# Kernel tuning notes

Measured on AMD Instinct MI355X. Metric: run time of the kernel, lower is better.

The kernel has to match this reference:

```python
import jax, jax.numpy as jnp
import numpy as np

T = 10          # time_steps
IN_DIM = 784    # 28*28
HID = 256
NCLS = 47
THRESH = 1.0
TAU_MEM = 2.0   # LIF membrane time constant
TAU_OUT = 2.0   # readout EMA time constant


@jax.custom_vjp
def spike_fn(u):
    # Heaviside spike on (v - threshold), surrogate gradient in bwd.
    return (u >= 0.0).astype(u.dtype)

def _spike_fwd(u):
    return spike_fn(u), u

def _spike_bwd(u, g):
    # sigmoid surrogate derivative, slope 4
    s = jax.nn.sigmoid(4.0 * u)
    return (g * 4.0 * s * (1.0 - s),)

spike_fn.defvjp(_spike_fwd, _spike_bwd)


def setup_inputs() -> dict:
    key = jax.random.key(0)
    k1, k2, k3 = jax.random.split(key, 3)
    x = jax.random.uniform(k1, (4096, 1, 28, 28), dtype=jnp.float32)
    W1 = jax.random.normal(k2, (IN_DIM, HID), dtype=jnp.float32) / np.float32(np.sqrt(IN_DIM))
    b1 = jnp.zeros((HID,), jnp.float32)
    Wr = jax.random.normal(k3, (HID, NCLS), dtype=jnp.float32) / np.float32(np.sqrt(HID))
    br = jnp.zeros((NCLS,), jnp.float32)
    return {"x": x, "W1": W1, "b1": b1, "Wr": Wr, "br": br}


def reference(x, W1, b1, Wr, br):
    B = x.shape[0]
    xf = x.reshape(B, -1)  # [B, 784] pixel intensities in [0,1]
    # rate_encode_flat: Bernoulli(p=pixel) spikes per timestep -> [T, B, 784]
    ek = jax.random.key(42)
    seq = (jax.random.uniform(ek, (T, B, IN_DIM), dtype=xf.dtype) < xf[None]).astype(xf.dtype)

    def step(carry, s_t):
        v_hid, v_out = carry
        I_hid = s_t @ W1 + b1                      # [B, HID]
        v_hid = v_hid + (I_hid - v_hid) / TAU_MEM  # leaky integration
        spk = spike_fn(v_hid - THRESH)             # spike emission
        v_hid = v_hid * (1.0 - spk)                # hard reset to 0
        I = spk @ Wr + br                          # [B, NCLS]
        v_out = v_out + (I - v_out) / TAU_OUT      # output EMA
        return (v_hid, v_out), None

    init = (jnp.zeros((B, HID), xf.dtype), jnp.zeros((B, NCLS), xf.dtype))
    (_, v_out), _ = jax.lax.scan(step, init, seq)
    return v_out
```

## Files before the change

kernel.cpp:

```cpp
#include <hip/hip_runtime.h>
#include <stdint.h>


#define T_STEPS 10
#define BATCH   4096
#define IN_DIM  784
#define HID     256
#define NCLS    47
#define NROWS   (T_STEPS * BATCH)
#define KWORDS  25
#define KPAD    800
#define M_TILE  160

#define WS_IALL_OFF 0u
#define WS_SPK_OFF  41943040u
#define WS_W1HI_OFF 46039040u
#define WS_W1MD_OFF (46039040u + 409600u)
#define WS_W1LO_OFF (46039040u + 819200u)

typedef __attribute__((ext_vector_type(8))) short    bf16x8;
typedef __attribute__((ext_vector_type(4))) float    f32x4;
typedef __attribute__((ext_vector_type(4))) uint32_t u32x4;

__device__ __forceinline__ uint32_t rotl32(uint32_t x, uint32_t r) {
    return __builtin_amdgcn_alignbit(x, x, 32u - r);
}

__device__ __forceinline__ uint32_t tf_hash(uint32_t lo) {
    const uint32_t ks1 = 42u;
    const uint32_t ks2 = 0x1BD11BDAu ^ 42u;
    uint32_t x0 = 0u;
    uint32_t x1 = lo + ks1;
#define TF_RND(r) { x0 += x1; x1 = rotl32(x1, r); x1 ^= x0; }
    TF_RND(13) TF_RND(15) TF_RND(26) TF_RND(6)
    x0 += ks1; x1 += ks2 + 1u;
    TF_RND(17) TF_RND(29) TF_RND(16) TF_RND(24)
    x0 += ks2; x1 += 2u;
    TF_RND(13) TF_RND(15) TF_RND(26) TF_RND(6)
    x1 += ks1 + 3u;
    TF_RND(17) TF_RND(29) TF_RND(16) TF_RND(24)
    x0 += ks1; x1 += ks2 + 4u;
    TF_RND(13) TF_RND(15) TF_RND(26) TF_RND(6)
    x0 += ks2; x1 += 5u;
#undef TF_RND
    return x0 ^ x1;
}

__global__ __launch_bounds__(256) void splitk_k(
        const float* __restrict__ W1, ushort* __restrict__ hiT,
        ushort* __restrict__ midT, ushort* __restrict__ loT) {
    int n = blockIdx.x;
    for (int k = threadIdx.x; k < KPAD; k += 256) {
        float w = (k < IN_DIM) ? W1[k * HID + n] : 0.0f;
        uint32_t u = __float_as_uint(w);
        uint32_t hb = (u + 0x7FFFu + ((u >> 16) & 1u)) >> 16;
        float hf = __uint_as_float(hb << 16);
        float r1 = w - hf;
        uint32_t u1 = __float_as_uint(r1);
        uint32_t mb = (u1 + 0x7FFFu + ((u1 >> 16) & 1u)) >> 16;
        float mf2 = __uint_as_float(mb << 16);
        float r2 = r1 - mf2;
        uint32_t u2 = __float_as_uint(r2);
        uint32_t lb = (u2 + 0x7FFFu + ((u2 >> 16) & 1u)) >> 16;
        hiT [n * KPAD + k] = (ushort)hb;
        midT[n * KPAD + k] = (ushort)mb;
        loT [n * KPAD + k] = (ushort)lb;
    }
}

__global__ __launch_bounds__(256) void spikegen_k(
        const float* __restrict__ x, uint32_t* __restrict__ spk) {
    const int kw  = blockIdx.y;
    const int row = (blockIdx.x << 8) + threadIdx.x;
    const int b   = row & (BATCH - 1);
    const int k0  = kw << 5;
    const float* xp = x + (size_t)b * IN_DIM + k0;
    const uint32_t ib = (uint32_t)row * (uint32_t)IN_DIM + (uint32_t)k0;
    uint32_t wbits = 0u;
#define SPIKE_G(g) { \
    float4 xa = *(const float4*)(xp + ((g) << 3)); \
    float4 xb = *(const float4*)(xp + ((g) << 3) + 4); \
    uint32_t base = ib + (uint32_t)((g) << 3); \
    uint32_t bits = 0u; \
    bits |= ((float)(tf_hash(base + 0u) >> 9) < xa.x * 8388608.0f) ? 1u   : 0u; \
    bits |= ((float)(tf_hash(base + 1u) >> 9) < xa.y * 8388608.0f) ? 2u   : 0u; \
    bits |= ((float)(tf_hash(base + 2u) >> 9) < xa.z * 8388608.0f) ? 4u   : 0u; \
    bits |= ((float)(tf_hash(base + 3u) >> 9) < xa.w * 8388608.0f) ? 8u   : 0u; \
    bits |= ((float)(tf_hash(base + 4u) >> 9) < xb.x * 8388608.0f) ? 16u  : 0u; \
    bits |= ((float)(tf_hash(base + 5u) >> 9) < xb.y * 8388608.0f) ? 32u  : 0u; \
    bits |= ((float)(tf_hash(base + 6u) >> 9) < xb.z * 8388608.0f) ? 64u  : 0u; \
    bits |= ((float)(tf_hash(base + 7u) >> 9) < xb.w * 8388608.0f) ? 128u : 0u; \
    wbits |= bits << ((g) << 3); }
    if (kw != KWORDS - 1) {
        SPIKE_G(0) SPIKE_G(1) SPIKE_G(2) SPIKE_G(3)
    } else {
        SPIKE_G(0) SPIKE_G(1)
    }
#undef SPIKE_G
    spk[(size_t)kw * NROWS + row] = wbits;
}

#define LDS_AB0 0
#define LDS_B0  20480
#define B_BUFSZ 49152
#define A_BUFSZ 10240

__global__ __launch_bounds__(512, 2) void fused_gemm_k(
        const ushort* __restrict__ hiT, const ushort* __restrict__ midT,
        const ushort* __restrict__ loT, const float* __restrict__ b1,
        const uint32_t* __restrict__ spk, float* __restrict__ I_all) {
    __shared__ __align__(16) char lds[118784];

    const int tid = threadIdx.x;
    const int l   = tid & 63;
    const int wv  = tid >> 6;
    const int wm  = wv >> 2;
    const int wn  = wv & 3;
    const int m0  = blockIdx.x * M_TILE;

    f32x4 acc[5][4] = {};

    const int q   = l >> 4;
    const int sig = q ^ (l & 3) ^ ((l >> 2) & 3);
    const int a_rd = wm * 5120 + ((l & 15) << 6) + (sig << 4);
    const int b_rd = (((wn << 6) + (l & 15)) << 6) + (sig << 4);

    const ushort* hi_p[2];
    const ushort* md_p[2];
    const ushort* lo_p[2];
    int bdst[2];
#pragma unroll
    for (int i = 0; i < 2; ++i) {
        int s  = (i << 9) + tid;
        int n  = s >> 2;
        int qs = s & 3;
        int qd = qs ^ (n & 3) ^ ((n >> 2) & 3);
        size_t eoff = (size_t)n * KPAD + ((size_t)qd << 3);
        hi_p[i] = hiT  + eoff;
        md_p[i] = midT + eoff;
        lo_p[i] = loT  + eoff;
        bdst[i] = ((i << 9) + (wv << 6)) << 4;
    }

    const int  eq   = tid & 3;
    const int  r1   = tid >> 2;
    const bool has2 = (tid < 128);
    const int  r2   = 128 + (tid >> 2);
    const int  ea1  = (r1 << 6) + ((eq ^ (r1 & 3) ^ ((r1 >> 2) & 3)) << 4);
    const int  ea2  = (r2 << 6) + ((eq ^ (r2 & 3) ^ ((r2 >> 2) & 3)) << 4);

    const uint32_t* sp1 = spk + (size_t)(m0 + r1);
    const uint32_t* sp2 = spk + (size_t)(m0 + (has2 ? r2 : r1));

#define SPIKE_FRAG_STORE(byt, dst) { \
    u32x4 v_; \
    v_.x = (((byt) & 1u)   ? 0x3F80u : 0u) | (((byt) & 2u)   ? 0x3F800000u : 0u); \
    v_.y = (((byt) & 4u)   ? 0x3F80u : 0u) | (((byt) & 8u)   ? 0x3F800000u : 0u); \
    v_.z = (((byt) & 16u)  ? 0x3F80u : 0u) | (((byt) & 32u)  ? 0x3F800000u : 0u); \
    v_.w = (((byt) & 64u)  ? 0x3F80u : 0u) | (((byt) & 128u) ? 0x3F800000u : 0u); \
    *(u32x4*)(dst) = v_; }

#define STAGE_B(koff, bbase) \
    _Pragma("unroll") \
    for (int i = 0; i < 2; ++i) { \
        __builtin_amdgcn_global_load_lds( \
            (const __attribute__((address_space(1))) void*)(hi_p[i] + (koff)), \
            (__attribute__((address_space(3))) void*)(lds + (bbase) + bdst[i]), \
            16, 0, 0); \
        __builtin_amdgcn_global_load_lds( \
            (const __attribute__((address_space(1))) void*)(md_p[i] + (koff)), \
            (__attribute__((address_space(3))) void*)(lds + (bbase) + 16384 + bdst[i]), \
            16, 0, 0); \
        __builtin_amdgcn_global_load_lds( \
            (const __attribute__((address_space(1))) void*)(lo_p[i] + (koff)), \
            (__attribute__((address_space(3))) void*)(lds + (bbase) + 32768 + bdst[i]), \
            16, 0, 0); \
    }

    uint32_t w1c = sp1[0];
    uint32_t w2c = has2 ? sp2[0] : 0u;
    STAGE_B(0, LDS_B0)
    SPIKE_FRAG_STORE((w1c >> (eq << 3)) & 0xffu, lds + ea1)
    if (has2) SPIKE_FRAG_STORE((w2c >> (eq << 3)) & 0xffu, lds + ea2)
    uint32_t w1n = sp1[NROWS];
    uint32_t w2n = has2 ? sp2[NROWS] : 0u;
    __syncthreads();

    int cur = 0;
#pragma unroll 1
    for (int kw = 0; kw < KWORDS; ++kw) {
        const int nxt = cur ^ 1;
        if (kw < KWORDS - 1) {
            const int koff = (kw + 1) << 5;
            STAGE_B(koff, LDS_B0 + nxt * B_BUFSZ)
            SPIKE_FRAG_STORE((w1n >> (eq << 3)) & 0xffu,
                             lds + nxt * A_BUFSZ + ea1)
            if (has2) SPIKE_FRAG_STORE((w2n >> (eq << 3)) & 0xffu,
                                       lds + nxt * A_BUFSZ + ea2)
            if (kw < KWORDS - 2) {
                w1n = sp1[(size_t)(kw + 2) * NROWS];
                if (has2) w2n = sp2[(size_t)(kw + 2) * NROWS];
            }
        }

        const char* A = lds + cur * A_BUFSZ;
        const char* B = lds + LDS_B0 + cur * B_BUFSZ;
        bf16x8 af[5];
#pragma unroll
        for (int mt = 0; mt < 5; ++mt)
            af[mt] = *(const bf16x8*)(A + a_rd + (mt << 10));
#pragma unroll
        for (int nt = 0; nt < 4; ++nt) {
            bf16x8 bh = *(const bf16x8*)(B + b_rd + (nt << 10));
            bf16x8 bm = *(const bf16x8*)(B + 16384 + b_rd + (nt << 10));
            bf16x8 bl = *(const bf16x8*)(B + 32768 + b_rd + (nt << 10));
#pragma unroll
            for (int mt = 0; mt < 5; ++mt) {
                acc[mt][nt] = __builtin_amdgcn_mfma_f32_16x16x32_bf16(af[mt], bh, acc[mt][nt], 0, 0, 0);
                acc[mt][nt] = __builtin_amdgcn_mfma_f32_16x16x32_bf16(af[mt], bm, acc[mt][nt], 0, 0, 0);
                acc[mt][nt] = __builtin_amdgcn_mfma_f32_16x16x32_bf16(af[mt], bl, acc[mt][nt], 0, 0, 0);
            }
        }

        __syncthreads();
        cur = nxt;
    }
#undef STAGE_B
#undef SPIKE_FRAG_STORE

    const int c0 = l & 15;
    float b1v[4];
#pragma unroll
    for (int nt = 0; nt < 4; ++nt)
        b1v[nt] = b1[(wn << 6) + (nt << 4) + c0];
#pragma unroll
    for (int mt = 0; mt < 5; ++mt) {
#pragma unroll
        for (int nt = 0; nt < 4; ++nt) {
            int col = (wn << 6) + (nt << 4) + c0;
#pragma unroll
            for (int r = 0; r < 4; ++r) {
                int row = m0 + wm * 80 + (mt << 4) + (q << 2) + r;
                I_all[(size_t)row * HID + col] = acc[mt][nt][r] + b1v[nt];
            }
        }
    }
}

__global__ __launch_bounds__(256) void scanout_k(
        const float* __restrict__ I_all, const float* __restrict__ Wr,
        const float* __restrict__ br, float* __restrict__ out) {
    __shared__ float gl[4 * 256];
    const int tid = threadIdx.x;
    const int b0  = blockIdx.x << 2;

#pragma unroll
    for (int b = 0; b < 4; ++b) {
        const float* p = I_all + ((size_t)(b0 + b) << 8) + tid;
        float v = 0.f, ga = 0.f, wt = 0.0009765625f;
#pragma unroll
        for (int t = 0; t < T_STEPS; ++t) {
            float I = p[(size_t)t * BATCH * HID];
            v = v + (I - v) * 0.5f;
            if (v >= 1.0f) { ga += wt; v = 0.f; }
            wt += wt;
        }
        gl[(b << 8) + tid] = ga;
    }
    __syncthreads();

    const int wv = tid >> 6;
    const int c  = tid & 63;
    if (c >= NCLS) return;
    const float* gb = &gl[wv << 8];
    float acc = 0.f;
    for (int h4 = 0; h4 < 64; ++h4) {
        float w0 = Wr[((h4 << 2) + 0) * NCLS + c];
        float w1 = Wr[((h4 << 2) + 1) * NCLS + c];
        float w2 = Wr[((h4 << 2) + 2) * NCLS + c];
        float w3 = Wr[((h4 << 2) + 3) * NCLS + c];
        float4 gg = *(const float4*)&gb[h4 << 2];
        acc = fmaf(gg.x, w0, acc);
        acc = fmaf(gg.y, w1, acc);
        acc = fmaf(gg.z, w2, acc);
        acc = fmaf(gg.w, w3, acc);
    }
    float brv = br[c] * 0.9990234375f;
    out[(b0 + wv) * NCLS + c] = acc + brv;
}

extern "C" void kernel_launch(void* const* d_in, const int* in_sizes, int n_in,
                              void* d_out, int out_size, void* d_ws, size_t ws_size,
                              hipStream_t stream) {
    const float* x  = (const float*)d_in[0];
    const float* W1 = (const float*)d_in[1];
    const float* b1 = (const float*)d_in[2];
    const float* Wr = (const float*)d_in[3];
    const float* br = (const float*)d_in[4];
    float* out = (float*)d_out;

    float*    I_all = (float*)   ((char*)d_ws + WS_IALL_OFF);
    uint32_t* spkw  = (uint32_t*)((char*)d_ws + WS_SPK_OFF);
    ushort*   w1hi  = (ushort*)  ((char*)d_ws + WS_W1HI_OFF);
    ushort*   w1md  = (ushort*)  ((char*)d_ws + WS_W1MD_OFF);
    ushort*   w1lo  = (ushort*)  ((char*)d_ws + WS_W1LO_OFF);

    splitk_k<<<HID, 256, 0, stream>>>(W1, w1hi, w1md, w1lo);
    spikegen_k<<<dim3(NROWS / 256, KWORDS), 256, 0, stream>>>(x, spkw);
    fused_gemm_k<<<NROWS / M_TILE, 512, 0, stream>>>(w1hi, w1md, w1lo, b1, spkw, I_all);
    scanout_k<<<BATCH / 4, 256, 0, stream>>>(I_all, Wr, br, out);
}
```

Measured before the change: 192.0 us.

## Fuse Bernoulli spike generation into the GEMM kernel, dropping spikegen pass

Removes the separate spike-generation kernel and its packed-bitmask workspace. Each GEMM thread now computes the Threefry hash for its 8-element spike fragment inline while staging the next K-slice. This saves a kernel launch and the global write and read of the spike words. In exchange, the hash ALU work is interleaved with the MFMA loop, which can lengthen the critical path and raise register pressure in the GEMM.

```diff
diff --git a/kernel.cpp b/kernel.cpp
--- a/kernel.cpp
+++ b/kernel.cpp
@@ -13,7 +13,6 @@
 #define M_TILE  160
 
 #define WS_IALL_OFF 0u
-#define WS_SPK_OFF  41943040u
 #define WS_W1HI_OFF 46039040u
 #define WS_W1MD_OFF (46039040u + 409600u)
 #define WS_W1LO_OFF (46039040u + 819200u)
@@ -44,6 +43,21 @@
     x0 += ks2; x1 += 5u;
 #undef TF_RND
     return x0 ^ x1;
+}
+
+__device__ __forceinline__ uint32_t hash8(uint32_t ib, const float* xp) {
+    float4 xa = *(const float4*)xp;
+    float4 xb = *(const float4*)(xp + 4);
+    uint32_t bits = 0u;
+    bits |= ((float)(tf_hash(ib + 0u) >> 9) < xa.x * 8388608.0f) ? 1u   : 0u;
+    bits |= ((float)(tf_hash(ib + 1u) >> 9) < xa.y * 8388608.0f) ? 2u   : 0u;
+    bits |= ((float)(tf_hash(ib + 2u) >> 9) < xa.z * 8388608.0f) ? 4u   : 0u;
+    bits |= ((float)(tf_hash(ib + 3u) >> 9) < xa.w * 8388608.0f) ? 8u   : 0u;
+    bits |= ((float)(tf_hash(ib + 4u) >> 9) < xb.x * 8388608.0f) ? 16u  : 0u;
+    bits |= ((float)(tf_hash(ib + 5u) >> 9) < xb.y * 8388608.0f) ? 32u  : 0u;
+    bits |= ((float)(tf_hash(ib + 6u) >> 9) < xb.z * 8388608.0f) ? 64u  : 0u;
+    bits |= ((float)(tf_hash(ib + 7u) >> 9) < xb.w * 8388608.0f) ? 128u : 0u;
+    return bits;
 }
 
 __global__ __launch_bounds__(256) void splitk_k(
@@ -68,39 +82,6 @@
     }
 }
 
-__global__ __launch_bounds__(256) void spikegen_k(
-        const float* __restrict__ x, uint32_t* __restrict__ spk) {
-    const int kw  = blockIdx.y;
-    const int row = (blockIdx.x << 8) + threadIdx.x;
-    const int b   = row & (BATCH - 1);
-    const int k0  = kw << 5;
-    const float* xp = x + (size_t)b * IN_DIM + k0;
-    const uint32_t ib = (uint32_t)row * (uint32_t)IN_DIM + (uint32_t)k0;
-    uint32_t wbits = 0u;
-#define SPIKE_G(g) { \
-    float4 xa = *(const float4*)(xp + ((g) << 3)); \
-    float4 xb = *(const float4*)(xp + ((g) << 3) + 4); \
-    uint32_t base = ib + (uint32_t)((g) << 3); \
-    uint32_t bits = 0u; \
-    bits |= ((float)(tf_hash(base + 0u) >> 9) < xa.x * 8388608.0f) ? 1u   : 0u; \
-    bits |= ((float)(tf_hash(base + 1u) >> 9) < xa.y * 8388608.0f) ? 2u   : 0u; \
-    bits |= ((float)(tf_hash(base + 2u) >> 9) < xa.z * 8388608.0f) ? 4u   : 0u; \
-    bits |= ((float)(tf_hash(base + 3u) >> 9) < xa.w * 8388608.0f) ? 8u   : 0u; \
-    bits |= ((float)(tf_hash(base + 4u) >> 9) < xb.x * 8388608.0f) ? 16u  : 0u; \
-    bits |= ((float)(tf_hash(base + 5u) >> 9) < xb.y * 8388608.0f) ? 32u  : 0u; \
-    bits |= ((float)(tf_hash(base + 6u) >> 9) < xb.z * 8388608.0f) ? 64u  : 0u; \
-    bits |= ((float)(tf_hash(base + 7u) >> 9) < xb.w * 8388608.0f) ? 128u : 0u; \
-    wbits |= bits << ((g) << 3); }
-    if (kw != KWORDS - 1) {
-        SPIKE_G(0) SPIKE_G(1) SPIKE_G(2) SPIKE_G(3)
-    } else {
-        SPIKE_G(0) SPIKE_G(1)
-    }
-#undef SPIKE_G
-    spk[(size_t)kw * NROWS + row] = wbits;
-}
-
-#define LDS_AB0 0
 #define LDS_B0  20480
 #define B_BUFSZ 49152
 #define A_BUFSZ 10240
@@ -108,7 +89,7 @@
 __global__ __launch_bounds__(512, 2) void fused_gemm_k(
         const ushort* __restrict__ hiT, const ushort* __restrict__ midT,
         const ushort* __restrict__ loT, const float* __restrict__ b1,
-        const uint32_t* __restrict__ spk, float* __restrict__ I_all) {
+        const float* __restrict__ x, float* __restrict__ I_all) {
     __shared__ __align__(16) char lds[118784];
 
     const int tid = threadIdx.x;
@@ -149,8 +130,12 @@
     const int  ea1  = (r1 << 6) + ((eq ^ (r1 & 3) ^ ((r1 >> 2) & 3)) << 4);
     const int  ea2  = (r2 << 6) + ((eq ^ (r2 & 3) ^ ((r2 >> 2) & 3)) << 4);
 
-    const uint32_t* sp1 = spk + (size_t)(m0 + r1);
-    const uint32_t* sp2 = spk + (size_t)(m0 + (has2 ? r2 : r1));
+    const int rg1 = m0 + r1;
+    const int rg2 = m0 + (has2 ? r2 : r1);
+    const float*   xp1 = x + (size_t)(rg1 & (BATCH - 1)) * IN_DIM + (eq << 3);
+    const float*   xp2 = x + (size_t)(rg2 & (BATCH - 1)) * IN_DIM + (eq << 3);
+    const uint32_t ib1 = (uint32_t)rg1 * (uint32_t)IN_DIM + (uint32_t)(eq << 3);
+    const uint32_t ib2 = (uint32_t)rg2 * (uint32_t)IN_DIM + (uint32_t)(eq << 3);
 
 #define SPIKE_FRAG_STORE(byt, dst) { \
     u32x4 v_; \
@@ -177,13 +162,15 @@
             16, 0, 0); \
     }
 
-    uint32_t w1c = sp1[0];
-    uint32_t w2c = has2 ? sp2[0] : 0u;
     STAGE_B(0, LDS_B0)
-    SPIKE_FRAG_STORE((w1c >> (eq << 3)) & 0xffu, lds + ea1)
-    if (has2) SPIKE_FRAG_STORE((w2c >> (eq << 3)) & 0xffu, lds + ea2)
-    uint32_t w1n = sp1[NROWS];
-    uint32_t w2n = has2 ? sp2[NROWS] : 0u;
+    {
+        uint32_t byt1 = hash8(ib1, xp1);
+        SPIKE_FRAG_STORE(byt1, lds + ea1)
+        if (has2) {
+            uint32_t byt2 = hash8(ib2, xp2);
+            SPIKE_FRAG_STORE(byt2, lds + ea2)
+        }
+    }
     __syncthreads();
 
     int cur = 0;
@@ -193,14 +180,14 @@
         if (kw < KWORDS - 1) {
             const int koff = (kw + 1) << 5;
             STAGE_B(koff, LDS_B0 + nxt * B_BUFSZ)
-            SPIKE_FRAG_STORE((w1n >> (eq << 3)) & 0xffu,
-                             lds + nxt * A_BUFSZ + ea1)
-            if (has2) SPIKE_FRAG_STORE((w2n >> (eq << 3)) & 0xffu,
-                                       lds + nxt * A_BUFSZ + ea2)
-            if (kw < KWORDS - 2) {
-                w1n = sp1[(size_t)(kw + 2) * NROWS];
-                if (has2) w2n = sp2[(size_t)(kw + 2) * NROWS];
+            const bool tail = (kw + 1 == KWORDS - 1);
+            uint32_t byt1 = 0u, byt2 = 0u;
+            if (!(tail && eq >= 2)) {
+                byt1 = hash8(ib1 + koff, xp1 + koff);
+                if (has2) byt2 = hash8(ib2 + koff, xp2 + koff);
             }
+            SPIKE_FRAG_STORE(byt1, lds + nxt * A_BUFSZ + ea1)
+            if (has2) SPIKE_FRAG_STORE(byt2, lds + nxt * A_BUFSZ + ea2)
         }
 
         const char* A = lds + cur * A_BUFSZ;
@@ -299,14 +286,12 @@
     const float* br = (const float*)d_in[4];
     float* out = (float*)d_out;
 
-    float*    I_all = (float*)   ((char*)d_ws + WS_IALL_OFF);
-    uint32_t* spkw  = (uint32_t*)((char*)d_ws + WS_SPK_OFF);
-    ushort*   w1hi  = (ushort*)  ((char*)d_ws + WS_W1HI_OFF);
-    ushort*   w1md  = (ushort*)  ((char*)d_ws + WS_W1MD_OFF);
-    ushort*   w1lo  = (ushort*)  ((char*)d_ws + WS_W1LO_OFF);
+    float*  I_all = (float*) ((char*)d_ws + WS_IALL_OFF);
+    ushort* w1hi  = (ushort*)((char*)d_ws + WS_W1HI_OFF);
+    ushort* w1md  = (ushort*)((char*)d_ws + WS_W1MD_OFF);
+    ushort* w1lo  = (ushort*)((char*)d_ws + WS_W1LO_OFF);
 
     splitk_k<<<HID, 256, 0, stream>>>(W1, w1hi, w1md, w1lo);
-    spikegen_k<<<dim3(NROWS / 256, KWORDS), 256, 0, stream>>>(x, spkw);
-    fused_gemm_k<<<NROWS / M_TILE, 512, 0, stream>>>(w1hi, w1md, w1lo, b1, spkw, I_all);
+    fused_gemm_k<<<NROWS / M_TILE, 512, 0, stream>>>(w1hi, w1md, w1lo, b1, x, I_all);
     scanout_k<<<BATCH / 4, 256, 0, stream>>>(I_all, Wr, br, out);
 }
```

Measured after the change: 197.0 us. 1.03x slower.
